# Performance work log

Measured on AMD Instinct MI355X. Metric: run time of the kernel, lower is better.

## Reference

```python
import jax, jax.numpy as jnp
import numpy as np
from jax import lax

H = 16  # hidden size

def lstm_dir(x_tbd, Wih, Whh, bih, bhh):
    # x_tbd: [T, B, D] -> outputs [T, B, H], final h [B, H]
    T, B, _ = x_tbd.shape
    xg = jnp.einsum('tbd,gd->tbg', x_tbd, Wih) + bih + bhh  # [T, B, 4H]
    def step(carry, xt):
        h, c = carry
        g = xt + h @ Whh.T
        i, f, gg, o = jnp.split(g, 4, axis=-1)  # PyTorch gate order i,f,g,o
        i = jax.nn.sigmoid(i); f = jax.nn.sigmoid(f)
        gg = jnp.tanh(gg); o = jax.nn.sigmoid(o)
        c = f * c + i * gg
        h = o * jnp.tanh(c)
        return (h, c), h
    init = (jnp.zeros((B, H), x_tbd.dtype), jnp.zeros((B, H), x_tbd.dtype))
    (hT, cT), hs = lax.scan(step, init, xg)
    return hs, hT

def bi_layer(x_tbd, pf, pb):
    hs_f, hT_f = lstm_dir(x_tbd, *pf)
    hs_b_rev, hT_b = lstm_dir(x_tbd[::-1], *pb)
    out = jnp.concatenate([hs_f, hs_b_rev[::-1]], axis=-1)  # [T, B, 2H]
    return out, hT_f, hT_b


def setup_inputs() -> dict:
    key = jax.random.key(0)
    ks = iter(jax.random.split(key, 32))
    B, T = 4096, 512
    d = {"x": jax.random.normal(next(ks), (B, T), jnp.float32)}
    def w(shape):
        return jax.random.normal(next(ks), shape, jnp.float32) * 0.2
    # layer 0 (input dim 1), forward / backward directions
    for s in ('f', 'b'):
        d[f'Wih0{s}'] = w((4 * H, 1)); d[f'Whh0{s}'] = w((4 * H, H))
        d[f'bih0{s}'] = jnp.zeros((4 * H,), jnp.float32)
        d[f'bhh0{s}'] = jnp.zeros((4 * H,), jnp.float32)
    # layer 1 (input dim 2H = 32)
    for s in ('f', 'b'):
        d[f'Wih1{s}'] = w((4 * H, 2 * H)); d[f'Whh1{s}'] = w((4 * H, H))
        d[f'bih1{s}'] = jnp.zeros((4 * H,), jnp.float32)
        d[f'bhh1{s}'] = jnp.zeros((4 * H,), jnp.float32)
    # MLP head: Linear(32,25), Linear(25,20)
    d['W1'] = w((25, 2 * H)); d['b1'] = jnp.zeros((25,), jnp.float32)
    d['W2'] = w((20, 25)); d['b2'] = jnp.zeros((20,), jnp.float32)
    return d


def reference(x, Wih0f, Whh0f, bih0f, bhh0f, Wih0b, Whh0b, bih0b, bhh0b,
              Wih1f, Whh1f, bih1f, bhh1f, Wih1b, Whh1b, bih1b, bhh1b,
              W1, b1, W2, b2):
    # x: [B, T] -> unsqueeze(2) -> [B, T, 1]; scan over time, so transpose to [T, B, 1]
    x_tbd = x.T[:, :, None]
    o0, _, _ = bi_layer(x_tbd, (Wih0f, Whh0f, bih0f, bhh0f), (Wih0b, Whh0b, bih0b, bhh0b))
    # dropout=0.1 between layers is inactive in eval mode (reference = eval)
    _, hT_f, hT_b = bi_layer(o0, (Wih1f, Whh1f, bih1f, bhh1f), (Wih1b, Whh1b, bih1b, bhh1b))
    # torch: cat((h[-1], h[-2]), 1) = (last-layer backward, last-layer forward)
    feat = jnp.concatenate([hT_b, hT_f], axis=1)  # [B, 32]
    z = jax.nn.elu(feat)
    z = jax.nn.elu(z @ W1.T + b1)
    z = jax.nn.elu(z @ W2.T + b2)
    return z  # [B, 20]
```

## Files before the change

kernel.cpp:

```cpp
#include <hip/hip_runtime.h>
#include <stdint.h>

#define TT 512
#define BB 4096
#define NT8 512
#define LOG2E 1.4426950408889634f

typedef _Float16 half8_t __attribute__((ext_vector_type(8)));
typedef __fp16 fp16x2_t __attribute__((ext_vector_type(2)));
typedef float f32x4 __attribute__((ext_vector_type(4)));
typedef float f32x2 __attribute__((ext_vector_type(2)));

union FragU { uint4 u4; half8_t h8; };
union PkU { fp16x2_t h2; unsigned int u; };

__device__ __forceinline__ float rcp_(float x){ return __builtin_amdgcn_rcpf(x); }
__device__ __forceinline__ float exp2_(float x){ return __builtin_amdgcn_exp2f(x); }
__device__ __forceinline__ float elu_(float x){ return x > 0.0f ? x : (exp2_(x * LOG2E) - 1.0f); }
__device__ __forceinline__ int mini_(int a, int b){ return a < b ? a : b; }
__device__ __forceinline__ float maskhi_(float x){ return __uint_as_float(__float_as_uint(x) & 0xFFFFE000u); }
__device__ __forceinline__ unsigned int pkrtz_(float a, float b){
    PkU p; p.h2 = __builtin_amdgcn_cvt_pkrtz(a, b); return p.u;
}
__device__ __forceinline__ unsigned int pkrne_(float a, float b){
    PkU p; p.h2[0] = (__fp16)a; p.h2[1] = (__fp16)b; return p.u;
}

__device__ __forceinline__ f32x4 MFMA(half8_t a, half8_t b, f32x4 c) {
    return __builtin_amdgcn_mfma_f32_16x16x32_f16(a, b, c, 0, 0, 0);
}

__device__ __forceinline__ f32x4 ld4_(const float* p){ return *(const f32x4*)p; }

__device__ __forceinline__ half8_t packA8s(const float* s, float sc) {
    half8_t h;
#pragma unroll
    for (int k = 0; k < 8; ++k) h[k] = (_Float16)(s[k] * sc);
    return h;
}
__device__ __forceinline__ half8_t zero8_() {
    half8_t h;
#pragma unroll
    for (int k = 0; k < 8; ++k) h[k] = (_Float16)0.0f;
    return h;
}

__device__ __forceinline__ void cell2p_(f32x2 gi, f32x2 gf, f32x2 gg, f32x2 go,
                                        f32x2& c, f32x2& h) {
    f32x2 ei, ef, eg, eo;
    ei[0] = exp2_(-gi[0]); ei[1] = exp2_(-gi[1]);
    ef[0] = exp2_(-gf[0]); ef[1] = exp2_(-gf[1]);
    eg[0] = exp2_(-gg[0]); eg[1] = exp2_(-gg[1]);
    eo[0] = exp2_(-go[0]); eo[1] = exp2_(-go[1]);
    const f32x2 one = {1.0f, 1.0f};
    f32x2 ai = one + ei, af = one + ef, ag = one + eg, ao = one + eo;
    f32x2 pif = ai * af, pgo = ag * ao;
    f32x2 P = pif * pgo;
    f32x2 R; R[0] = rcp_(P[0]); R[1] = rcp_(P[1]);
    f32x2 I = R * (af * pgo);
    f32x2 F = R * (ai * pgo);
    f32x2 Gt = R * (pif * ao);
    f32x2 O = R * (pif * ag);
    f32x2 G = Gt + Gt - one;
    c = F * c + I * G;
    f32x2 ct = c * (-2.0f * LOG2E);
    f32x2 et; et[0] = exp2_(ct[0]); et[1] = exp2_(ct[1]);
    f32x2 den = one + et;
    f32x2 Rt; Rt[0] = rcp_(den[0]); Rt[1] = rcp_(den[1]);
    f32x2 T = Rt + Rt - one;
    h = O * T;
}


struct PA {
    const float *x;
    const float *WihF, *WhhF, *bihF, *bhhF;
    const float *WihB, *WhhB, *bihB, *bhhB;
    char* ws;
};

__global__ __launch_bounds__(256) void phaseA_k(PA p) {
    const int tid = threadIdx.x;
    const int lane = tid & 63;
    const int wv   = tid >> 6;
    const int q = lane >> 4, b = lane & 15, c = b & 7;
    const bool hi8 = b >= 8;
    const int chain = blockIdx.x * 4 + wv;
    const int tile = chain >> 1, dir = chain & 1;

    const float* Wih = dir ? p.WihB : p.WihF;
    const float* Whh = dir ? p.WhhB : p.WhhF;
    const float* bih = dir ? p.bihB : p.bihF;
    const float* bhh = dir ? p.bhhB : p.bhhF;

    auto mkA = [&](int m, float sc)->half8_t {
        if (q < 2) return packA8s(Whh + (16*m + b)*16 + 8*q, sc);
        half8_t h = zero8_();
        if (q == 2) {
            float w = Wih[16*m + b] * sc;
            h[0] = (_Float16)w;
            h[1] = (_Float16)w;
        }
        return h;
    };
    half8_t A0 = mkA(0, LOG2E);
    half8_t A1 = mkA(1, LOG2E);
    half8_t A2 = mkA(2, 2.0f*LOG2E);
    half8_t A3 = mkA(3, LOG2E);

    f32x4 bias0 = (ld4_(bih +      4*q) + ld4_(bhh +      4*q)) * LOG2E;
    f32x4 bias1 = (ld4_(bih + 16 + 4*q) + ld4_(bhh + 16 + 4*q)) * LOG2E;
    f32x4 bias2 = (ld4_(bih + 32 + 4*q) + ld4_(bhh + 32 + 4*q)) * (2.0f*LOG2E);
    f32x4 bias3 = (ld4_(bih + 48 + 4*q) + ld4_(bhh + 48 + 4*q)) * LOG2E;

    const int uu = 4*q + (hi8 ? 2 : 0);
    const int sa0 = 32*(q&1) + c;
    const int sa1 = sa0 + 8;
    const int sa2 = sa0 + 16;
    const int sa3 = sa0 + 24;
    const bool qlt2 = q < 2;
    const bool q2   = q == 2;

    unsigned int hh = 0u;
    f32x2 cc = {0.f, 0.f};

    const char* xbase = (const char*)p.x + (size_t)tile*8*TT*4;
    const int   xoff  = c*TT*4;
    char*       wsbase = p.ws + (size_t)tile*TT*512;
    const int   woff  = c*64 + dir*32 + uu*2;

    auto xld = [&](int s_)->float {
        int s = mini_(s_, TT-1);
        int t = dir ? (TT-1-s) : s;
        return *(const float*)(xbase + (size_t)t*4 + xoff);
    };

    auto step = [&](float xv, int t) {
        float mh = maskhi_(xv);
        unsigned int xp = pkrtz_(mh, xv - mh);
        unsigned int s0 = (unsigned int)__shfl((int)hh, sa0);
        unsigned int s1 = (unsigned int)__shfl((int)hh, sa1);
        unsigned int s2 = (unsigned int)__shfl((int)hh, sa2);
        unsigned int s3 = (unsigned int)__shfl((int)hh, sa3);
        FragU hf;
        hf.u4.x = qlt2 ? s0 : (q2 ? xp : 0u);
        hf.u4.y = qlt2 ? s1 : 0u;
        hf.u4.z = qlt2 ? s2 : 0u;
        hf.u4.w = qlt2 ? s3 : 0u;
        f32x4 r0 = MFMA(A0, hf.h8, bias0);
        f32x4 r1 = MFMA(A1, hf.h8, bias1);
        f32x4 r2 = MFMA(A2, hf.h8, bias2);
        f32x4 r3 = MFMA(A3, hf.h8, bias3);
        f32x2 gi, gf, gg, go;
        gi[0] = hi8 ? r0[2] : r0[0]; gi[1] = hi8 ? r0[3] : r0[1];
        gf[0] = hi8 ? r1[2] : r1[0]; gf[1] = hi8 ? r1[3] : r1[1];
        gg[0] = hi8 ? r2[2] : r2[0]; gg[1] = hi8 ? r2[3] : r2[1];
        go[0] = hi8 ? r3[2] : r3[0]; go[1] = hi8 ? r3[3] : r3[1];
        f32x2 hv;
        cell2p_(gi, gf, gg, go, cc, hv);
        hh = pkrne_(hv[0], hv[1]);
        *(unsigned int*)(wsbase + (size_t)t*512 + woff) = hh;
    };

    float xv0 = xld(0), xv1 = xld(1), xv2 = xld(2), xv3 = xld(3);
    for (int s = 0; s < TT; s += 4) {
        const int t0 = dir ? (TT-1-s) : s;
        const int d  = dir ? -1 : 1;
        step(xv0, t0      ); xv0 = xld(s+4);
        step(xv1, t0 + d  ); xv1 = xld(s+5);
        step(xv2, t0 + 2*d); xv2 = xld(s+6);
        step(xv3, t0 + 3*d); xv3 = xld(s+7);
    }
}

struct PB {
    const float *WihF, *WhhF, *bihF, *bhhF;
    const float *WihB, *WhhB, *bihB, *bhhB;
    const char* ws;
    float* hT;
};

__global__ __launch_bounds__(256) void phaseB_k(PB p) {
    __shared__ uint4 ldsAll[4 * 16];
    const int tid = threadIdx.x;
    const int lane = tid & 63;
    const int wv   = tid >> 6;
    char* lds = (char*)ldsAll + wv * 256;
    const int q = lane >> 4, b = lane & 15, c = b & 7;
    const bool hi8 = b >= 8;
    const int chain = blockIdx.x * 4 + wv;
    const int tile = chain >> 1, dir = chain & 1;

    const float* Wih = dir ? p.WihB : p.WihF;
    const float* Whh = dir ? p.WhhB : p.WhhF;
    const float* bih = dir ? p.bihB : p.bihF;
    const float* bhh = dir ? p.bhhB : p.bhhF;

    const float SC0 = LOG2E, SC1 = LOG2E, SC2 = 2.0f*LOG2E, SC3 = LOG2E;

    half8_t wi0 = packA8s(Wih + (     b)*32 + 8*q, SC0);
    half8_t wi1 = packA8s(Wih + (16 + b)*32 + 8*q, SC1);
    half8_t wi2 = packA8s(Wih + (32 + b)*32 + 8*q, SC2);
    half8_t wi3 = packA8s(Wih + (48 + b)*32 + 8*q, SC3);

    half8_t wh0 = (q < 2) ? packA8s(Whh + (     b)*16 + 8*q, SC0) : zero8_();
    half8_t wh1 = (q < 2) ? packA8s(Whh + (16 + b)*16 + 8*q, SC1) : zero8_();
    half8_t wh2 = (q < 2) ? packA8s(Whh + (32 + b)*16 + 8*q, SC2) : zero8_();
    half8_t wh3 = (q < 2) ? packA8s(Whh + (48 + b)*16 + 8*q, SC3) : zero8_();

    f32x4 bias0 = (ld4_(bih +      4*q) + ld4_(bhh +      4*q)) * SC0;
    f32x4 bias1 = (ld4_(bih + 16 + 4*q) + ld4_(bhh + 16 + 4*q)) * SC1;
    f32x4 bias2 = (ld4_(bih + 32 + 4*q) + ld4_(bhh + 32 + 4*q)) * SC2;
    f32x4 bias3 = (ld4_(bih + 48 + 4*q) + ld4_(bhh + 48 + 4*q)) * SC3;

    const int uu  = 4*q + (hi8 ? 2 : 0);
    const int who = c*32 + uu*2;
    const int rdo = c*32 + (q&1)*16;

    ((unsigned int*)lds)[lane & 63] = 0u;
    __builtin_amdgcn_wave_barrier();

    f32x2 cc = {0.f, 0.f};
    f32x2 hv = {0.f, 0.f};

    const char* wsbase = p.ws + (size_t)tile*TT*512;
    const int   xoff   = c*64 + q*16;

    auto xld = [&](int s_)->uint4 {
        int s = mini_(s_, TT-1);
        int t = dir ? (TT-1-s) : s;
        return *(const uint4*)(wsbase + (size_t)t*512 + xoff);
    };

    auto wiM = [&](uint4 xin, f32x4& o0, f32x4& o1, f32x4& o2, f32x4& o3) {
        FragU xf; xf.u4 = xin;
        o0 = MFMA(wi0, xf.h8, bias0);
        o1 = MFMA(wi1, xf.h8, bias1);
        o2 = MFMA(wi2, xf.h8, bias2);
        o3 = MFMA(wi3, xf.h8, bias3);
    };

    auto stepWh = [&](f32x4 p0, f32x4 p1, f32x4 p2, f32x4 p3) {
        FragU hf; hf.u4 = *(const uint4*)(lds + rdo);
        f32x4 r0 = MFMA(wh0, hf.h8, p0);
        f32x4 r1 = MFMA(wh1, hf.h8, p1);
        f32x4 r2 = MFMA(wh2, hf.h8, p2);
        f32x4 r3 = MFMA(wh3, hf.h8, p3);
        f32x2 gi, gf, gg, go;
        gi[0] = hi8 ? r0[2] : r0[0]; gi[1] = hi8 ? r0[3] : r0[1];
        gf[0] = hi8 ? r1[2] : r1[0]; gf[1] = hi8 ? r1[3] : r1[1];
        gg[0] = hi8 ? r2[2] : r2[0]; gg[1] = hi8 ? r2[3] : r2[1];
        go[0] = hi8 ? r3[2] : r3[0]; go[1] = hi8 ? r3[3] : r3[1];
        cell2p_(gi, gf, gg, go, cc, hv);
        unsigned int hh = pkrne_(hv[0], hv[1]);
        *(unsigned int*)(lds + who) = hh;
        __builtin_amdgcn_wave_barrier();
    };

    uint4 xb0 = xld(0), xb1 = xld(1), xb2 = xld(2), xb3 = xld(3);
    f32x4 pa0, pa1, pa2, pa3, pb0, pb1, pb2, pb3;
    wiM(xb0, pa0, pa1, pa2, pa3);
    for (int s = 0; s < TT; s += 4) {
        wiM(xb1, pb0, pb1, pb2, pb3);
        stepWh(pa0, pa1, pa2, pa3);
        xb0 = xld(s+4);
        wiM(xb2, pa0, pa1, pa2, pa3);
        stepWh(pb0, pb1, pb2, pb3);
        xb1 = xld(s+5);
        wiM(xb3, pb0, pb1, pb2, pb3);
        stepWh(pa0, pa1, pa2, pa3);
        xb2 = xld(s+6);
        wiM(xb0, pa0, pa1, pa2, pa3);
        stepWh(pb0, pb1, pb2, pb3);
        xb3 = xld(s+7);
    }

    const int batch = tile*8 + c;
    float* hp = p.hT + ((size_t)(dir ? BB : 0) + batch)*16 + uu;
    float2 ho; ho.x = hv[0]; ho.y = hv[1];
    *(float2*)hp = ho;
}

struct PC {
    const float* hT;
    const float *W1, *b1, *W2, *b2;
    float* out;
};

__global__ __launch_bounds__(64) void head_k(PC p) {
    const int B = blockIdx.x * 64 + threadIdx.x;
    const float* hf = p.hT + (size_t)B*16;
    const float* hb = p.hT + ((size_t)BB + B)*16;

    float z0[32];
#pragma unroll
    for (int k = 0; k < 16; ++k) z0[k] = elu_(hb[k]);
#pragma unroll
    for (int k = 0; k < 16; ++k) z0[16+k] = elu_(hf[k]);

    float z1[25];
#pragma unroll
    for (int o = 0; o < 25; ++o) {
        float a = p.b1[o];
#pragma unroll
        for (int k = 0; k < 32; ++k) a = fmaf(p.W1[o*32 + k], z0[k], a);
        z1[o] = elu_(a);
    }
#pragma unroll
    for (int o = 0; o < 20; ++o) {
        float a = p.b2[o];
#pragma unroll
        for (int k = 0; k < 25; ++k) a = fmaf(p.W2[o*25 + k], z1[k], a);
        p.out[(size_t)B*20 + o] = elu_(a);
    }
}

extern "C" void kernel_launch(void* const* d_in, const int* in_sizes, int n_in,
                              void* d_out, int out_size, void* d_ws, size_t ws_size,
                              hipStream_t stream) {
    (void)in_sizes; (void)n_in; (void)out_size;

    const size_t frag_bytes = (size_t)NT8 * TT * 512;
    const size_t hT_bytes   = (size_t)2 * BB * 16 * sizeof(float);
    size_t hT_off = (ws_size >= frag_bytes + hT_bytes) ? frag_bytes
                                                       : (ws_size - hT_bytes);
    char* ws = (char*)d_ws;
    float* hT = (float*)(ws + hT_off);

    PA pa;
    pa.x = (const float*)d_in[0];
    pa.WihF = (const float*)d_in[1];  pa.WhhF = (const float*)d_in[2];
    pa.bihF = (const float*)d_in[3];  pa.bhhF = (const float*)d_in[4];
    pa.WihB = (const float*)d_in[5];  pa.WhhB = (const float*)d_in[6];
    pa.bihB = (const float*)d_in[7];  pa.bhhB = (const float*)d_in[8];
    pa.ws = ws;
    hipLaunchKernelGGL(phaseA_k, dim3(256), dim3(256), 0, stream, pa);

    PB pb;
    pb.WihF = (const float*)d_in[9];   pb.WhhF = (const float*)d_in[10];
    pb.bihF = (const float*)d_in[11];  pb.bhhF = (const float*)d_in[12];
    pb.WihB = (const float*)d_in[13];  pb.WhhB = (const float*)d_in[14];
    pb.bihB = (const float*)d_in[15];  pb.bhhB = (const float*)d_in[16];
    pb.ws = ws; pb.hT = hT;
    hipLaunchKernelGGL(phaseB_k, dim3(256), dim3(256), 0, stream, pb);

    PC pc;
    pc.hT = hT;
    pc.W1 = (const float*)d_in[17]; pc.b1 = (const float*)d_in[18];
    pc.W2 = (const float*)d_in[19]; pc.b2 = (const float*)d_in[20];
    pc.out = (float*)d_out;
    hipLaunchKernelGGL(head_k, dim3(BB/64), dim3(64), 0, stream, pc);
}
```

Measured before the change: 286.7 us.

## Use 16x16x16 MFMA for recurrent step with xor-shuffle h exchange

Both phases switch the recurrent h·Whh product from a padded 16x16x32 MFMA to a 16x16x16 MFMA. The B fragment is built with a single xor-8 shuffle, replacing four shuffles in phase A and the LDS store/load round trip with wave barrier in phase B. Phase A also drops the fp16 hi/lo split of the scalar x input. It now folds Wih*x into the accumulator init with fp32 FMAs, pipelined one step ahead. The aim is to shorten the serial per-step latency chain, with some risk if the shuffle layout mapping is wrong.

```diff
diff --git a/kernel.cpp b/kernel.cpp
--- a/kernel.cpp
+++ b/kernel.cpp
@@ -7,27 +7,28 @@
 #define LOG2E 1.4426950408889634f
 
 typedef _Float16 half8_t __attribute__((ext_vector_type(8)));
+typedef _Float16 half4_t __attribute__((ext_vector_type(4)));
 typedef __fp16 fp16x2_t __attribute__((ext_vector_type(2)));
 typedef float f32x4 __attribute__((ext_vector_type(4)));
 typedef float f32x2 __attribute__((ext_vector_type(2)));
 
-union FragU { uint4 u4; half8_t h8; };
+union FragU  { uint4 u4; half8_t h8; };
+union Frag2U { uint2 u2; half4_t h4; };
 union PkU { fp16x2_t h2; unsigned int u; };
 
 __device__ __forceinline__ float rcp_(float x){ return __builtin_amdgcn_rcpf(x); }
 __device__ __forceinline__ float exp2_(float x){ return __builtin_amdgcn_exp2f(x); }
 __device__ __forceinline__ float elu_(float x){ return x > 0.0f ? x : (exp2_(x * LOG2E) - 1.0f); }
 __device__ __forceinline__ int mini_(int a, int b){ return a < b ? a : b; }
-__device__ __forceinline__ float maskhi_(float x){ return __uint_as_float(__float_as_uint(x) & 0xFFFFE000u); }
-__device__ __forceinline__ unsigned int pkrtz_(float a, float b){
-    PkU p; p.h2 = __builtin_amdgcn_cvt_pkrtz(a, b); return p.u;
-}
 __device__ __forceinline__ unsigned int pkrne_(float a, float b){
     PkU p; p.h2[0] = (__fp16)a; p.h2[1] = (__fp16)b; return p.u;
 }
 
-__device__ __forceinline__ f32x4 MFMA(half8_t a, half8_t b, f32x4 c) {
+__device__ __forceinline__ f32x4 MFMA32(half8_t a, half8_t b, f32x4 c) {
     return __builtin_amdgcn_mfma_f32_16x16x32_f16(a, b, c, 0, 0, 0);
+}
+__device__ __forceinline__ f32x4 MFMA16(half4_t a, half4_t b, f32x4 c) {
+    return __builtin_amdgcn_mfma_f32_16x16x16f16(a, b, c, 0, 0, 0);
 }
 
 __device__ __forceinline__ f32x4 ld4_(const float* p){ return *(const f32x4*)p; }
@@ -38,10 +39,10 @@
     for (int k = 0; k < 8; ++k) h[k] = (_Float16)(s[k] * sc);
     return h;
 }
-__device__ __forceinline__ half8_t zero8_() {
-    half8_t h;
-#pragma unroll
-    for (int k = 0; k < 8; ++k) h[k] = (_Float16)0.0f;
+__device__ __forceinline__ half4_t packA4s(const float* s, float sc) {
+    half4_t h;
+#pragma unroll
+    for (int k = 0; k < 4; ++k) h[k] = (_Float16)(s[k] * sc);
     return h;
 }
 
@@ -93,34 +94,24 @@
     const float* bih = dir ? p.bihB : p.bihF;
     const float* bhh = dir ? p.bhhB : p.bhhF;
 
-    auto mkA = [&](int m, float sc)->half8_t {
-        if (q < 2) return packA8s(Whh + (16*m + b)*16 + 8*q, sc);
-        half8_t h = zero8_();
-        if (q == 2) {
-            float w = Wih[16*m + b] * sc;
-            h[0] = (_Float16)w;
-            h[1] = (_Float16)w;
-        }
-        return h;
-    };
-    half8_t A0 = mkA(0, LOG2E);
-    half8_t A1 = mkA(1, LOG2E);
-    half8_t A2 = mkA(2, 2.0f*LOG2E);
-    half8_t A3 = mkA(3, LOG2E);
-
-    f32x4 bias0 = (ld4_(bih +      4*q) + ld4_(bhh +      4*q)) * LOG2E;
-    f32x4 bias1 = (ld4_(bih + 16 + 4*q) + ld4_(bhh + 16 + 4*q)) * LOG2E;
-    f32x4 bias2 = (ld4_(bih + 32 + 4*q) + ld4_(bhh + 32 + 4*q)) * (2.0f*LOG2E);
-    f32x4 bias3 = (ld4_(bih + 48 + 4*q) + ld4_(bhh + 48 + 4*q)) * LOG2E;
+    const float SC0 = LOG2E, SC1 = LOG2E, SC2 = 2.0f*LOG2E, SC3 = LOG2E;
+
+    half4_t A0 = packA4s(Whh + (     b)*16 + 4*q, SC0);
+    half4_t A1 = packA4s(Whh + (16 + b)*16 + 4*q, SC1);
+    half4_t A2 = packA4s(Whh + (32 + b)*16 + 4*q, SC2);
+    half4_t A3 = packA4s(Whh + (48 + b)*16 + 4*q, SC3);
+
+    f32x4 bias0 = (ld4_(bih +      4*q) + ld4_(bhh +      4*q)) * SC0;
+    f32x4 bias1 = (ld4_(bih + 16 + 4*q) + ld4_(bhh + 16 + 4*q)) * SC1;
+    f32x4 bias2 = (ld4_(bih + 32 + 4*q) + ld4_(bhh + 32 + 4*q)) * SC2;
+    f32x4 bias3 = (ld4_(bih + 48 + 4*q) + ld4_(bhh + 48 + 4*q)) * SC3;
+
+    f32x4 wihx0 = ld4_(Wih +      4*q) * SC0;
+    f32x4 wihx1 = ld4_(Wih + 16 + 4*q) * SC1;
+    f32x4 wihx2 = ld4_(Wih + 32 + 4*q) * SC2;
+    f32x4 wihx3 = ld4_(Wih + 48 + 4*q) * SC3;
 
     const int uu = 4*q + (hi8 ? 2 : 0);
-    const int sa0 = 32*(q&1) + c;
-    const int sa1 = sa0 + 8;
-    const int sa2 = sa0 + 16;
-    const int sa3 = sa0 + 24;
-    const bool qlt2 = q < 2;
-    const bool q2   = q == 2;
-
     unsigned int hh = 0u;
     f32x2 cc = {0.f, 0.f};
 
@@ -135,22 +126,22 @@
         return *(const float*)(xbase + (size_t)t*4 + xoff);
     };
 
-    auto step = [&](float xv, int t) {
-        float mh = maskhi_(xv);
-        unsigned int xp = pkrtz_(mh, xv - mh);
-        unsigned int s0 = (unsigned int)__shfl((int)hh, sa0);
-        unsigned int s1 = (unsigned int)__shfl((int)hh, sa1);
-        unsigned int s2 = (unsigned int)__shfl((int)hh, sa2);
-        unsigned int s3 = (unsigned int)__shfl((int)hh, sa3);
-        FragU hf;
-        hf.u4.x = qlt2 ? s0 : (q2 ? xp : 0u);
-        hf.u4.y = qlt2 ? s1 : 0u;
-        hf.u4.z = qlt2 ? s2 : 0u;
-        hf.u4.w = qlt2 ? s3 : 0u;
-        f32x4 r0 = MFMA(A0, hf.h8, bias0);
-        f32x4 r1 = MFMA(A1, hf.h8, bias1);
-        f32x4 r2 = MFMA(A2, hf.h8, bias2);
-        f32x4 r3 = MFMA(A3, hf.h8, bias3);
+    auto mkCin = [&](float xv, f32x4& o0, f32x4& o1, f32x4& o2, f32x4& o3) {
+        o0 = bias0 + wihx0 * xv;
+        o1 = bias1 + wihx1 * xv;
+        o2 = bias2 + wihx2 * xv;
+        o3 = bias3 + wihx3 * xv;
+    };
+
+    auto step = [&](f32x4 p0, f32x4 p1, f32x4 p2, f32x4 p3, int t) {
+        unsigned int swp = (unsigned int)__shfl_xor((int)hh, 8);
+        Frag2U bf;
+        bf.u2.x = hi8 ? swp : hh;
+        bf.u2.y = hi8 ? hh : swp;
+        f32x4 r0 = MFMA16(A0, bf.h4, p0);
+        f32x4 r1 = MFMA16(A1, bf.h4, p1);
+        f32x4 r2 = MFMA16(A2, bf.h4, p2);
+        f32x4 r3 = MFMA16(A3, bf.h4, p3);
         f32x2 gi, gf, gg, go;
         gi[0] = hi8 ? r0[2] : r0[0]; gi[1] = hi8 ? r0[3] : r0[1];
         gf[0] = hi8 ? r1[2] : r1[0]; gf[1] = hi8 ? r1[3] : r1[1];
@@ -163,13 +154,19 @@
     };
 
     float xv0 = xld(0), xv1 = xld(1), xv2 = xld(2), xv3 = xld(3);
+    f32x4 ca0, ca1, ca2, ca3, cb0, cb1, cb2, cb3;
+    mkCin(xv0, ca0, ca1, ca2, ca3);
     for (int s = 0; s < TT; s += 4) {
         const int t0 = dir ? (TT-1-s) : s;
         const int d  = dir ? -1 : 1;
-        step(xv0, t0      ); xv0 = xld(s+4);
-        step(xv1, t0 + d  ); xv1 = xld(s+5);
-        step(xv2, t0 + 2*d); xv2 = xld(s+6);
-        step(xv3, t0 + 3*d); xv3 = xld(s+7);
+        mkCin(xv1, cb0, cb1, cb2, cb3);
+        step(ca0, ca1, ca2, ca3, t0);        xv0 = xld(s+4);
+        mkCin(xv2, ca0, ca1, ca2, ca3);
+        step(cb0, cb1, cb2, cb3, t0 + d);    xv1 = xld(s+5);
+        mkCin(xv3, cb0, cb1, cb2, cb3);
+        step(ca0, ca1, ca2, ca3, t0 + 2*d);  xv2 = xld(s+6);
+        mkCin(xv0, ca0, ca1, ca2, ca3);
+        step(cb0, cb1, cb2, cb3, t0 + 3*d);  xv3 = xld(s+7);
     }
 }
 
@@ -181,11 +178,9 @@
 };
 
 __global__ __launch_bounds__(256) void phaseB_k(PB p) {
-    __shared__ uint4 ldsAll[4 * 16];
     const int tid = threadIdx.x;
     const int lane = tid & 63;
     const int wv   = tid >> 6;
-    char* lds = (char*)ldsAll + wv * 256;
     const int q = lane >> 4, b = lane & 15, c = b & 7;
     const bool hi8 = b >= 8;
     const int chain = blockIdx.x * 4 + wv;
@@ -203,23 +198,18 @@
     half8_t wi2 = packA8s(Wih + (32 + b)*32 + 8*q, SC2);
     half8_t wi3 = packA8s(Wih + (48 + b)*32 + 8*q, SC3);
 
-    half8_t wh0 = (q < 2) ? packA8s(Whh + (     b)*16 + 8*q, SC0) : zero8_();
-    half8_t wh1 = (q < 2) ? packA8s(Whh + (16 + b)*16 + 8*q, SC1) : zero8_();
-    half8_t wh2 = (q < 2) ? packA8s(Whh + (32 + b)*16 + 8*q, SC2) : zero8_();
-    half8_t wh3 = (q < 2) ? packA8s(Whh + (48 + b)*16 + 8*q, SC3) : zero8_();
+    half4_t wh0 = packA4s(Whh + (     b)*16 + 4*q, SC0);
+    half4_t wh1 = packA4s(Whh + (16 + b)*16 + 4*q, SC1);
+    half4_t wh2 = packA4s(Whh + (32 + b)*16 + 4*q, SC2);
+    half4_t wh3 = packA4s(Whh + (48 + b)*16 + 4*q, SC3);
 
     f32x4 bias0 = (ld4_(bih +      4*q) + ld4_(bhh +      4*q)) * SC0;
     f32x4 bias1 = (ld4_(bih + 16 + 4*q) + ld4_(bhh + 16 + 4*q)) * SC1;
     f32x4 bias2 = (ld4_(bih + 32 + 4*q) + ld4_(bhh + 32 + 4*q)) * SC2;
     f32x4 bias3 = (ld4_(bih + 48 + 4*q) + ld4_(bhh + 48 + 4*q)) * SC3;
 
-    const int uu  = 4*q + (hi8 ? 2 : 0);
-    const int who = c*32 + uu*2;
-    const int rdo = c*32 + (q&1)*16;
-
-    ((unsigned int*)lds)[lane & 63] = 0u;
-    __builtin_amdgcn_wave_barrier();
-
+    const int uu = 4*q + (hi8 ? 2 : 0);
+    unsigned int hh = 0u;
     f32x2 cc = {0.f, 0.f};
     f32x2 hv = {0.f, 0.f};
 
@@ -234,27 +224,28 @@
 
     auto wiM = [&](uint4 xin, f32x4& o0, f32x4& o1, f32x4& o2, f32x4& o3) {
         FragU xf; xf.u4 = xin;
-        o0 = MFMA(wi0, xf.h8, bias0);
-        o1 = MFMA(wi1, xf.h8, bias1);
-        o2 = MFMA(wi2, xf.h8, bias2);
-        o3 = MFMA(wi3, xf.h8, bias3);
+        o0 = MFMA32(wi0, xf.h8, bias0);
+        o1 = MFMA32(wi1, xf.h8, bias1);
+        o2 = MFMA32(wi2, xf.h8, bias2);
+        o3 = MFMA32(wi3, xf.h8, bias3);
     };
 
     auto stepWh = [&](f32x4 p0, f32x4 p1, f32x4 p2, f32x4 p3) {
-        FragU hf; hf.u4 = *(const uint4*)(lds + rdo);
-        f32x4 r0 = MFMA(wh0, hf.h8, p0);
-        f32x4 r1 = MFMA(wh1, hf.h8, p1);
-        f32x4 r2 = MFMA(wh2, hf.h8, p2);
-        f32x4 r3 = MFMA(wh3, hf.h8, p3);
+        unsigned int swp = (unsigned int)__shfl_xor((int)hh, 8);
+        Frag2U bf;
+        bf.u2.x = hi8 ? swp : hh;
+        bf.u2.y = hi8 ? hh : swp;
+        f32x4 r0 = MFMA16(wh0, bf.h4, p0);
+        f32x4 r1 = MFMA16(wh1, bf.h4, p1);
+        f32x4 r2 = MFMA16(wh2, bf.h4, p2);
+        f32x4 r3 = MFMA16(wh3, bf.h4, p3);
         f32x2 gi, gf, gg, go;
         gi[0] = hi8 ? r0[2] : r0[0]; gi[1] = hi8 ? r0[3] : r0[1];
         gf[0] = hi8 ? r1[2] : r1[0]; gf[1] = hi8 ? r1[3] : r1[1];
         gg[0] = hi8 ? r2[2] : r2[0]; gg[1] = hi8 ? r2[3] : r2[1];
         go[0] = hi8 ? r3[2] : r3[0]; go[1] = hi8 ? r3[3] : r3[1];
         cell2p_(gi, gf, gg, go, cc, hv);
-        unsigned int hh = pkrne_(hv[0], hv[1]);
-        *(unsigned int*)(lds + who) = hh;
-        __builtin_amdgcn_wave_barrier();
+        hh = pkrne_(hv[0], hv[1]);
     };
 
     uint4 xb0 = xld(0), xb1 = xld(1), xb2 = xld(2), xb3 = xld(3);
```

Result: slower. 316.6 us (+10.4%).
